# Kernel tuning notes

Measured on AMD Instinct MI355X. Metric: run time of the kernel, lower is better.

## Reference

```python
import jax, jax.numpy as jnp
import numpy as np

# --- SLAYER params (nmnistNet.yaml) ---
THETA = 10.0
TS = 1.0
TAU_REF = 1.0
SCALE_REF = 2.0
T_SAMPLE = 300
B = 8

def _alpha_kernel(tau, mult, t_sample, ts, eps=0.01):
    vals = []
    t = 0.0
    while t < t_sample:
        v = mult * t / tau * np.exp(1.0 - t / tau)
        if abs(v) < eps and t > tau:
            break
        vals.append(v)
        t += ts
    return np.asarray(vals, np.float32)

# refractory kernel: alpha kernel with mult = -scaleRef*theta (slayer._calculateRefKernel)
REF_KERNEL = _alpha_kernel(TAU_REF, -SCALE_REF * THETA, T_SAMPLE, TS)
NREF = REF_KERNEL.shape[0]  # 11 for these params; REF_KERNEL[0] == 0


def spike(u):
    """slayerCuda.getSpikes: per-neuron sequential threshold recurrence over time.
    u: [..., T] membrane potential. On spike at t, REF_KERNEL is accumulated
    into u[t:t+NREF]; spike amplitude is 1/Ts."""
    uT = jnp.moveaxis(u, -1, 0)  # [T, ...]
    refk = jnp.asarray(REF_KERNEL[1:]).reshape((NREF - 1,) + (1,) * (u.ndim - 1))
    buf0 = jnp.zeros((NREF - 1,) + uT.shape[1:], u.dtype)  # pending refractory

    def step(buf, u_t):
        u_mod = u_t + buf[0]
        ev = (u_mod >= THETA).astype(u.dtype)
        buf = jnp.concatenate([buf[1:], jnp.zeros_like(buf[:1])], axis=0) + ev[None] * refk
        return buf, ev / TS

    _, s = jax.lax.scan(step, buf0, uT)
    return jnp.moveaxis(s, 0, -1)


def conv2d_t(x, w, pad):
    """slayer.conv: Conv3d with kernel (k,k,1) == per-timestep 2D conv.
    x: [B,C,H,W,T], w: [O,I,kh,kw]."""
    b, c, h, wd, t = x.shape
    xb = jnp.moveaxis(x, -1, 1).reshape(b * t, c, h, wd)
    y = jax.lax.conv_general_dilated(xb, w, (1, 1), [(pad, pad), (pad, pad)],
                                     dimension_numbers=('NCHW', 'OIHW', 'NCHW'))
    o, ho, wo = y.shape[1], y.shape[2], y.shape[3]
    return jnp.moveaxis(y.reshape(b, t, o, ho, wo), 1, -1)


def sum_pool2(x):
    """slayer.pool(2): fixed-weight (1.1*theta) 2x2/stride-2 sum over H,W per channel."""
    y = jax.lax.reduce_window(x, 0.0, jax.lax.add, (1, 1, 2, 2, 1), (1, 1, 2, 2, 1), 'VALID')
    return 1.1 * THETA * y


def setup_inputs():
    key = jax.random.key(0)
    k0, k1, k2, k3, k4 = jax.random.split(key, 5)
    spikeInput = (jax.random.uniform(k0, (B, 2, 34, 34, T_SAMPLE)) < 0.1).astype(jnp.float32) / TS
    # conv weights: kaiming-uniform bound * 100 (the __init__ scales conv weights by 100)
    w1 = jax.random.uniform(k1, (16, 2, 5, 5), minval=-14.1, maxval=14.1, dtype=jnp.float32)
    w2 = jax.random.uniform(k2, (32, 16, 3, 3), minval=-8.3, maxval=8.3, dtype=jnp.float32)
    w3 = jax.random.uniform(k3, (64, 32, 3, 3), minval=-5.9, maxval=5.9, dtype=jnp.float32)
    wfc = jax.random.uniform(k4, (10, 64, 8, 8), minval=-0.5, maxval=0.5, dtype=jnp.float32)
    return {"spikeInput": spikeInput, "w1": w1, "w2": w2, "w3": w3, "wfc": wfc}


def reference(spikeInput, w1, w2, w3, wfc):
    s1 = spike(conv2d_t(spikeInput, w1, 1))  # [B,16,32,32,T]
    s2 = spike(sum_pool2(s1))                # [B,16,16,16,T]
    s3 = spike(conv2d_t(s2, w2, 1))          # [B,32,16,16,T]
    s4 = spike(sum_pool2(s3))                # [B,32,8,8,T]
    s5 = spike(conv2d_t(s4, w3, 1))          # [B,64,8,8,T]
    # dense((8,8,64),10): Conv3d(64,10,(8,8,1)) == full-spatial contraction
    u = jnp.einsum('bchwt,ochw->bot', s5, wfc)[:, :, None, None, :]
    return spike(u)                          # [B,10,1,1,T]
```

## Files before the change

kernel.cpp:

```cpp
#include <hip/hip_runtime.h>
#include <hip/hip_bf16.h>
#include <cmath>

#define T_SAMPLE 300
#define NCHUNK 75

typedef __attribute__((ext_vector_type(8))) short short8;
typedef __attribute__((ext_vector_type(4))) float f32x4;

struct RefK { float v[10]; };

__device__ __forceinline__ unsigned char spike_step(float u, float* buf, const RefK& rk) {
    const float um = u + buf[0];
    const bool fire = um >= 10.0f;
    const float ev = fire ? 1.0f : 0.0f;
#pragma unroll
    for (int r = 0; r < 9; ++r) buf[r] = fmaf(ev, rk.v[r], buf[r + 1]);
    buf[9] = ev * rk.v[9];
    return fire ? (unsigned char)1 : (unsigned char)0;
}

__device__ __forceinline__ short8 bytes_to_bf16x8(uint2 w8) {
    union { uint4 u; short8 s8; } cv;
    cv.u.x = (w8.x & 0xFFu) * 0x3F80u | ((((w8.x >> 8) & 0xFFu) * 0x3F80u) << 16);
    cv.u.y = ((w8.x >> 16) & 0xFFu) * 0x3F80u | ((((w8.x >> 24) & 0xFFu) * 0x3F80u) << 16);
    cv.u.z = (w8.y & 0xFFu) * 0x3F80u | ((((w8.y >> 8) & 0xFFu) * 0x3F80u) << 16);
    cv.u.w = ((w8.y >> 16) & 0xFFu) * 0x3F80u | ((((w8.y >> 24) & 0xFFu) * 0x3F80u) << 16);
    return cv.s8;
}

__device__ __forceinline__ unsigned short bf16_split_sel(float w, int s) {
    __hip_bfloat16 hb = __float2bfloat16(w);
    const float hf = __bfloat162float(hb);
    __hip_bfloat16 mb = __float2bfloat16(w - hf);
    const float mf = __bfloat162float(mb);
    __hip_bfloat16 lb = __float2bfloat16(w - hf - mf);
    __hip_bfloat16 sel = (s == 0) ? hb : ((s == 1) ? mb : lb);
    return *(unsigned short*)&sel;
}

__global__ __launch_bounds__(256) void transpose_in_k(
    const float* __restrict__ In, unsigned int* __restrict__ X)
{
    __shared__ unsigned int lds[16 * NCHUNK];
    const int blk = blockIdx.x;
    const int tn = threadIdx.x >> 4;
    const int tq = threadIdx.x & 15;
    const size_t n = (size_t)blk * 16 + tn;
#pragma unroll
    for (int p = 0; p < 5; ++p) {
        const int ch = p * 16 + tq;
        if (ch < NCHUNK) {
            const float4 v = *(const float4*)(In + n * T_SAMPLE + ch * 4);
            unsigned int u = (v.x != 0.f ? 1u : 0u) | (v.y != 0.f ? 0x100u : 0u) |
                             (v.z != 0.f ? 0x10000u : 0u) | (v.w != 0.f ? 0x1000000u : 0u);
            lds[tn * NCHUNK + ch] = u;
        }
    }
    __syncthreads();
    for (int idx = threadIdx.x; idx < 16 * NCHUNK; idx += 256) {
        const int ch = idx >> 4, t2 = idx & 15;
        X[(size_t)ch * 18496 + blk * 16 + t2] = lds[t2 * NCHUNK + ch];
    }
}

__global__ __launch_bounds__(256) void prep_w1_k(
    const float* __restrict__ w1, unsigned short* __restrict__ Wr1)
{
    const int g = blockIdx.x * 256 + threadIdx.x;
    const int j = g & 7;
    const int lane = (g >> 3) & 63;
    const int ks = (g >> 9) & 3;
    const int s = g >> 11;
    const int q = lane >> 4;
    const int oc = lane & 15;
    const int kg = ks * 32 + q * 8 + j;
    const int slot = kg >> 2, c = kg & 1;
    const int dy = slot / 6, dx = slot % 6;
    const float w = (dy < 5 && dx < 5) ? w1[((oc * 2 + c) * 5 + dy) * 5 + dx] * 0.5f : 0.f;
    Wr1[g] = bf16_split_sel(w, s);
}

__global__ __launch_bounds__(256) void prep_w3_k(
    const float* __restrict__ w3, unsigned short* __restrict__ Wr)
{
    const int g = blockIdx.x * 256 + threadIdx.x;
    const int j = g & 7;
    const int lane = (g >> 3) & 63;
    const int mt = (g >> 9) & 3;
    const int rest = g >> 11;
    const int ks = rest % 9;
    const int s = rest / 9;
    const int oc = mt * 16 + (lane & 15);
    const int ic = (lane >> 4) * 8 + j;
    Wr[g] = bf16_split_sel(w3[(oc * 32 + ic) * 9 + ks], s);
}

__global__ __launch_bounds__(256) void prep_w2_k(
    const float* __restrict__ w2, unsigned short* __restrict__ Wr2)
{
    const int g = blockIdx.x * 256 + threadIdx.x;
    const int j = g & 7;
    const int lane = (g >> 3) & 63;
    const int mt = (g >> 9) & 1;
    const int rest = g >> 10;
    const int kp = rest % 5;
    const int s = rest / 5;
    const int q = lane >> 4;
    const int oc = mt * 16 + (lane & 15);
    const int tap = kp * 2 + (q >> 1);
    const int ic = (q & 1) * 8 + j;
    const float w = (tap <= 8) ? w2[(oc * 16 + ic) * 9 + tap] : 0.f;
    Wr2[g] = bf16_split_sel(w, s);
}

__device__ __forceinline__ void c1_mfma_chunk(
    const unsigned int* __restrict__ tb, const int* offA, const int* offB,
    const short8* Af, f32x4* acc)
{
    unsigned int vA[4][4], vB[4][4];
#pragma unroll
    for (int ks = 0; ks < 4; ++ks)
#pragma unroll
        for (int t = 0; t < 4; ++t) {
            vA[ks][t] = tb[t * 72 + offA[ks]];
            vB[ks][t] = tb[t * 72 + offB[ks]];
        }

#pragma unroll
    for (int t = 0; t < 4; ++t) acc[t] = (f32x4){0.f, 0.f, 0.f, 0.f};
#pragma unroll
    for (int ks = 0; ks < 4; ++ks)
#pragma unroll
        for (int t = 0; t < 4; ++t) {
            union { uint4 u; short8 s8; } cv;
            cv.u.x = vA[ks][t]; cv.u.y = vA[ks][t];
            cv.u.z = vB[ks][t]; cv.u.w = vB[ks][t];
#pragma unroll
            for (int s = 0; s < 3; ++s)
                acc[t] = __builtin_amdgcn_mfma_f32_16x16x32_bf16(
                    Af[s * 4 + ks], cv.s8, acc[t], 0, 0, 0);
        }
}

__device__ __forceinline__ void c1_spike_store(
    const f32x4* acc, float (*buf)[10], const RefK& rk,
    uchar4* __restrict__ S1, int ch, int nb0)
{
#pragma unroll
    for (int rr = 0; rr < 4; ++rr) {
        uchar4 o;
        o.x = spike_step(acc[0][rr], buf[rr], rk);
        o.y = spike_step(acc[1][rr], buf[rr], rk);
        o.z = spike_step(acc[2][rr], buf[rr], rk);
        o.w = spike_step(acc[3][rr], buf[rr], rk);
        S1[(size_t)ch * 131072 + nb0 + rr * 1024] = o;
    }
}

__global__ __launch_bounds__(64) void conv1sp_k(
    const unsigned int* __restrict__ X, const unsigned short* __restrict__ Wr1,
    uchar4* __restrict__ S1, RefK rk)
{
    __shared__ unsigned int tab[25 * 4 * 72];
    const int pg = blockIdx.x;
    const int b = blockIdx.y;
    const int ty = pg >> 2, tx = pg & 3;
    const int lane = threadIdx.x;
    const int q = lane >> 4, n = lane & 15;
    const int py0 = n >> 3, px0 = n & 7;

    short8 Af[12];
#pragma unroll
    for (int s = 0; s < 3; ++s)
#pragma unroll
        for (int ks = 0; ks < 4; ++ks)
            Af[s * 4 + ks] = *(const short8*)(Wr1 + (((s * 4 + ks) * 64 + lane) * 8));

    int offA[4], offB[4];
#pragma unroll
    for (int ks = 0; ks < 4; ++ks) {
        const int sA = ks * 8 + q * 2, sB = sA + 1;
        const int dyA = sA / 6, dxA = sA - dyA * 6;
        const int dyB = sB / 6, dxB = sB - dyB * 6;
        offA[ks] = min(py0 + dyA, 5) * 12 + min(px0 + dxA, 11);
        offB[ks] = min(py0 + dyB, 5) * 12 + min(px0 + dxB, 11);
    }

    int lidx[29];
    int gof[29];
#pragma unroll
    for (int i = 0; i < 29; ++i) {
        const int e = i * 64 + lane;
        if (e < 1800) {
            const int chl = e / 72, site = e - chl * 72;
            const int r = site / 12, cc = site - r * 12;
            const int gy = ty * 2 - 1 + r, gx = tx * 8 - 1 + cc;
            lidx[i] = chl * 288 + site;
            gof[i] = (((unsigned)gy < 34u) && ((unsigned)gx < 34u))
                   ? (chl * 18496 + (b * 2) * 1156 + gy * 34 + gx) : -1;
        } else { lidx[i] = -1; gof[i] = -1; }
    }

    unsigned int w0[29], w1[29];
#pragma unroll
    for (int i = 0; i < 29; ++i) {
        if (gof[i] >= 0) { w0[i] = X[gof[i]]; w1[i] = X[gof[i] + 1156]; }
        else { w0[i] = 0u; w1[i] = 0u; }
    }

    float buf[4][10];
#pragma unroll
    for (int rr = 0; rr < 4; ++rr)
#pragma unroll
        for (int r = 0; r < 10; ++r) buf[rr][r] = 0.f;

    const int nb0 = (b * 16 + q * 4) * 1024 + (ty * 2 + py0) * 32 + tx * 8 + px0;

    f32x4 accA[4], accB[4];

    for (int st = 0; st < 3; ++st) {
#pragma unroll
        for (int i = 0; i < 29; ++i) {
            if (lidx[i] >= 0) {
#pragma unroll
                for (int t = 0; t < 4; ++t)
                    tab[lidx[i] + t * 72] =
                        ((w0[i] >> (8 * t)) & 0xFFu) * 0x3F80u
                        | ((((w1[i] >> (8 * t)) & 0xFFu) * 0x3F80u) << 16);
            }
        }
        __syncthreads();

        if (st < 2) {
            const unsigned int* Xs = X + (size_t)(st + 1) * (25 * 18496);
#pragma unroll
            for (int i = 0; i < 29; ++i) {
                if (gof[i] >= 0) { w0[i] = Xs[gof[i]]; w1[i] = Xs[gof[i] + 1156]; }
            }
        }

        const int ch0 = st * 25;
        c1_mfma_chunk(tab, offA, offB, Af, accA);
        for (int pp = 0; pp < 12; ++pp) {
            c1_mfma_chunk(tab + (2 * pp + 1) * 288, offA, offB, Af, accB);
            c1_spike_store(accA, buf, rk, S1, ch0 + 2 * pp, nb0);
            c1_mfma_chunk(tab + (2 * pp + 2) * 288, offA, offB, Af, accA);
            c1_spike_store(accB, buf, rk, S1, ch0 + 2 * pp + 1, nb0);
        }
        c1_spike_store(accA, buf, rk, S1, ch0 + 24, nb0);
        __syncthreads();
    }
}

__global__ __launch_bounds__(256) void conv2_mfma_k(
    const unsigned int* __restrict__ s2u, const unsigned short* __restrict__ Wr2,
    float4* __restrict__ U, int b0, int nbl)
{
    __shared__ __align__(16) unsigned char pad[4 * 18 * 18 * 16];
    const int tc = blockIdx.x;
    const int bl = blockIdx.z;
    const int b = b0 + bl;
    const int tid = threadIdx.x;
    const int wv = tid >> 6, lane = tid & 63;
    const int q = lane >> 4, n = lane & 15;
    const int PLANE_U = nbl * 8192;

    unsigned int* lp = (unsigned int*)pad;
    for (int i = tid; i < 5184; i += 256) lp[i] = 0u;
    __syncthreads();
    const unsigned int* sb = s2u + (size_t)tc * 32768 + b * 4096;
    for (int e = tid; e < 4096; e += 256) {
        const unsigned int v = sb[e];
        const int c = e >> 8, pix = e & 255;
        const int base = (((pix >> 4) + 1) * 18 + ((pix & 15) + 1)) * 16 + c;
        pad[base]         = (unsigned char)(v & 0xFFu);
        pad[5184 + base]  = (unsigned char)((v >> 8) & 0xFFu);
        pad[10368 + base] = (unsigned char)((v >> 16) & 0xFFu);
        pad[15552 + base] = (unsigned char)(v >> 24);
    }
    __syncthreads();

    for (int i = 0; i < 4; ++i) {
        const int r = wv * 4 + i;
        f32x4 acc[2][4];
#pragma unroll
        for (int mt = 0; mt < 2; ++mt)
#pragma unroll
            for (int t = 0; t < 4; ++t) acc[mt][t] = (f32x4){0.f, 0.f, 0.f, 0.f};

        for (int kp = 0; kp < 5; ++kp) {
            short8 Af[6];
#pragma unroll
            for (int s = 0; s < 3; ++s)
#pragma unroll
                for (int mt = 0; mt < 2; ++mt)
                    Af[s * 2 + mt] = *(const short8*)(Wr2 + ((((s * 5 + kp) * 2 + mt) * 64 + lane) * 8));
            int tap = kp * 2 + (q >> 1);
            if (tap > 8) tap = 8;
            const int dy = tap / 3, dx = tap % 3;
#pragma unroll
            for (int t = 0; t < 4; ++t) {
                const int off = ((t * 18 + r + dy) * 18 + (n + dx)) * 16 + (q & 1) * 8;
                const short8 Bf = bytes_to_bf16x8(*(const uint2*)(pad + off));
#pragma unroll
                for (int s = 0; s < 3; ++s)
#pragma unroll
                    for (int mt = 0; mt < 2; ++mt)
                        acc[mt][t] = __builtin_amdgcn_mfma_f32_16x16x32_bf16(
                            Af[s * 2 + mt], Bf, acc[mt][t], 0, 0, 0);
            }
        }

        const size_t ub = (size_t)tc * PLANE_U;
#pragma unroll
        for (int mt = 0; mt < 2; ++mt)
#pragma unroll
            for (int rr = 0; rr < 4; ++rr) {
                const int oc = mt * 16 + q * 4 + rr;
                const int nb = (bl * 32 + oc) * 256 + r * 16 + n;
                U[ub + nb] = make_float4(acc[mt][0][rr], acc[mt][1][rr], acc[mt][2][rr], acc[mt][3][rr]);
            }
    }
}

__global__ __launch_bounds__(256) void conv3_mfma_k(
    const unsigned int* __restrict__ s4u, const unsigned short* __restrict__ Wr,
    float4* __restrict__ U)
{
    __shared__ __align__(16) unsigned char pad[12800];
    const int tc = blockIdx.x;
    const int bl = blockIdx.z;
    const int tid = threadIdx.x;
    const int wv = tid >> 6, lane = tid & 63;
    const int q = lane >> 4, n = lane & 15;

    unsigned int* lp = (unsigned int*)pad;
    for (int i = tid; i < 3200; i += 256) lp[i] = 0u;
    __syncthreads();
    const unsigned int* sb = s4u + (size_t)tc * 16384 + bl * 2048;
    for (int e = tid; e < 2048; e += 256) {
        const unsigned int v = sb[e];
        const int c = e >> 6, pix = e & 63;
        const int base = (((pix >> 3) + 1) * 10 + ((pix & 7) + 1)) * 32 + c;
        pad[base]        = (unsigned char)(v & 0xFFu);
        pad[3200 + base] = (unsigned char)((v >> 8) & 0xFFu);
        pad[6400 + base] = (unsigned char)((v >> 16) & 0xFFu);
        pad[9600 + base] = (unsigned char)(v >> 24);
    }
    __syncthreads();

    const int pixel = wv * 16 + n;
    const int py0 = pixel >> 3, px0 = pixel & 7;

    f32x4 acc[4][4];
#pragma unroll
    for (int mt = 0; mt < 4; ++mt)
#pragma unroll
        for (int t = 0; t < 4; ++t) acc[mt][t] = (f32x4){0.f, 0.f, 0.f, 0.f};

    for (int ks = 0; ks < 9; ++ks) {
        const int dy = ks / 3, dx = ks % 3;
        short8 Af[12];
#pragma unroll
        for (int s = 0; s < 3; ++s)
#pragma unroll
            for (int mt = 0; mt < 4; ++mt)
                Af[s * 4 + mt] = *(const short8*)(Wr + ((((s * 9 + ks) * 4 + mt) * 64 + lane) * 8));
#pragma unroll
        for (int t = 0; t < 4; ++t) {
            const int off = ((t * 10 + py0 + dy) * 10 + (px0 + dx)) * 32 + q * 8;
            const short8 Bf = bytes_to_bf16x8(*(const uint2*)(pad + off));
#pragma unroll
            for (int s = 0; s < 3; ++s)
#pragma unroll
                for (int mt = 0; mt < 4; ++mt)
                    acc[mt][t] = __builtin_amdgcn_mfma_f32_16x16x32_bf16(
                        Af[s * 4 + mt], Bf, acc[mt][t], 0, 0, 0);
        }
    }

    const size_t ub = (size_t)tc * 32768 + (size_t)bl * 4096;
#pragma unroll
    for (int mt = 0; mt < 4; ++mt)
#pragma unroll
        for (int r = 0; r < 4; ++r) {
            const int oc = mt * 16 + q * 4 + r;
            const int nb = oc * 64 + wv * 16 + n;
            U[ub + nb] = make_float4(acc[mt][0][r], acc[mt][1][r], acc[mt][2][r], acc[mt][3][r]);
        }
}

__device__ __forceinline__ void spike_body(
    const float4* __restrict__ U, uchar4* __restrict__ S,
    int nneur, int sstride, int soff, const RefK& rk)
{
    const int n = blockIdx.x * 64 + threadIdx.x;
    const float4* up = U + n;
    uchar4* sp = S + soff + n;
    float buf[10];
#pragma unroll
    for (int r = 0; r < 10; ++r) buf[r] = 0.f;

    float4 ring[8];
#pragma unroll
    for (int r = 0; r < 8; ++r) ring[r] = up[(size_t)r * nneur];

#pragma unroll 8
    for (int ch = 0; ch < 72; ++ch) {
        const float4 cur = ring[ch & 7];
        const int pf = (ch + 8 < NCHUNK) ? ch + 8 : NCHUNK - 1;
        ring[ch & 7] = up[(size_t)pf * nneur];
        uchar4 o;
        o.x = spike_step(cur.x, buf, rk);
        o.y = spike_step(cur.y, buf, rk);
        o.z = spike_step(cur.z, buf, rk);
        o.w = spike_step(cur.w, buf, rk);
        sp[(size_t)ch * sstride] = o;
    }
#pragma unroll
    for (int ch = 72; ch < NCHUNK; ++ch) {
        const float4 cur = ring[ch & 7];
        uchar4 o;
        o.x = spike_step(cur.x, buf, rk);
        o.y = spike_step(cur.y, buf, rk);
        o.z = spike_step(cur.z, buf, rk);
        o.w = spike_step(cur.w, buf, rk);
        sp[(size_t)ch * sstride] = o;
    }
}

__global__ __launch_bounds__(64) void spike2_k(
    const float4* U, uchar4* S, int nneur, int sstride, int soff, RefK rk)
{ spike_body(U, S, nneur, sstride, soff, rk); }

__global__ __launch_bounds__(64) void spike3_k(
    const float4* U, uchar4* S, int nneur, int sstride, int soff, RefK rk)
{ spike_body(U, S, nneur, sstride, soff, rk); }

__device__ __forceinline__ int bsum4(uint2 r0, uint2 r1, int k) {
    return (int)((r0.x >> (8 * k)) & 0xffu) + (int)((r0.y >> (8 * k)) & 0xffu)
         + (int)((r1.x >> (8 * k)) & 0xffu) + (int)((r1.y >> (8 * k)) & 0xffu);
}

template <int C, int H, int W>
__device__ __forceinline__ void pool_body(
    const uchar4* __restrict__ Sin, uchar4* __restrict__ Sout, const RefK& rk)
{
    constexpr int H2 = H / 2, W2 = W / 2;
    constexpr int SIN = 8 * C * H * W;
    constexpr int SOUT = 8 * C * H2 * W2;
    const int n = blockIdx.x * 64 + threadIdx.x;
    const int x = n % W2;
    const int y = (n / W2) % H2;
    const int c = (n / (W2 * H2)) % C;
    const int b = n / (W2 * H2 * C);
    const int base = (((b * C + c) * H + 2 * y) * W + 2 * x);
    uchar4* q = Sout + n;

    float buf[10];
#pragma unroll
    for (int r = 0; r < 10; ++r) buf[r] = 0.f;

    uint2 r0[8], r1[8];
#pragma unroll
    for (int r = 0; r < 8; ++r) {
        r0[r] = *(const uint2*)(Sin + (size_t)r * SIN + base);
        r1[r] = *(const uint2*)(Sin + (size_t)r * SIN + base + W);
    }

#pragma unroll 8
    for (int ch = 0; ch < 72; ++ch) {
        const uint2 a0 = r0[ch & 7], a1 = r1[ch & 7];
        const int pf = (ch + 8 < NCHUNK) ? ch + 8 : NCHUNK - 1;
        r0[ch & 7] = *(const uint2*)(Sin + (size_t)pf * SIN + base);
        r1[ch & 7] = *(const uint2*)(Sin + (size_t)pf * SIN + base + W);
        uchar4 o;
        o.x = spike_step(11.0f * (float)bsum4(a0, a1, 0), buf, rk);
        o.y = spike_step(11.0f * (float)bsum4(a0, a1, 1), buf, rk);
        o.z = spike_step(11.0f * (float)bsum4(a0, a1, 2), buf, rk);
        o.w = spike_step(11.0f * (float)bsum4(a0, a1, 3), buf, rk);
        q[(size_t)ch * SOUT] = o;
    }
#pragma unroll
    for (int ch = 72; ch < NCHUNK; ++ch) {
        const uint2 a0 = r0[ch & 7], a1 = r1[ch & 7];
        uchar4 o;
        o.x = spike_step(11.0f * (float)bsum4(a0, a1, 0), buf, rk);
        o.y = spike_step(11.0f * (float)bsum4(a0, a1, 1), buf, rk);
        o.z = spike_step(11.0f * (float)bsum4(a0, a1, 2), buf, rk);
        o.w = spike_step(11.0f * (float)bsum4(a0, a1, 3), buf, rk);
        q[(size_t)ch * SOUT] = o;
    }
}

__global__ __launch_bounds__(64) void pool2_k(
    const uchar4* Sin, uchar4* Sout, RefK rk) { pool_body<16, 32, 32>(Sin, Sout, rk); }
__global__ __launch_bounds__(64) void pool4_k(
    const uchar4* Sin, uchar4* Sout, RefK rk) { pool_body<32, 16, 16>(Sin, Sout, rk); }

__global__ __launch_bounds__(64) void dense_k(
    const uchar4* __restrict__ S5, const float* __restrict__ WFC,
    float4* __restrict__ U6)
{
    const int tc = blockIdx.x, o = blockIdx.y, b = blockIdx.z;
    const int lane = threadIdx.x;
    float a0 = 0.f, a1 = 0.f, a2 = 0.f, a3 = 0.f;
    const uchar4* sb = S5 + (size_t)tc * 32768 + b * 4096;
    const float* wb = WFC + o * 4096;
    for (int i = 0; i < 64; ++i) {
        const int site = i * 64 + lane;
        const uchar4 s = sb[site];
        const float w = wb[site];
        a0 = fmaf(w, (float)s.x, a0);
        a1 = fmaf(w, (float)s.y, a1);
        a2 = fmaf(w, (float)s.z, a2);
        a3 = fmaf(w, (float)s.w, a3);
    }
#pragma unroll
    for (int m = 1; m < 64; m <<= 1) {
        a0 += __shfl_xor(a0, m, 64);
        a1 += __shfl_xor(a1, m, 64);
        a2 += __shfl_xor(a2, m, 64);
        a3 += __shfl_xor(a3, m, 64);
    }
    if (lane == 0)
        U6[(size_t)tc * 80 + b * 10 + o] = make_float4(a0, a1, a2, a3);
}

__global__ __launch_bounds__(128) void spike6_k(
    const float4* __restrict__ U6, float* __restrict__ Out, RefK rk)
{
    const int n = threadIdx.x;
    if (n >= 80) return;
    const float4* up = U6 + n;
    float* op = Out + (size_t)n * T_SAMPLE;
    float buf[10];
#pragma unroll
    for (int r = 0; r < 10; ++r) buf[r] = 0.f;

    float4 ring[8];
#pragma unroll
    for (int r = 0; r < 8; ++r) ring[r] = up[(size_t)r * 80];

#pragma unroll 8
    for (int ch = 0; ch < 72; ++ch) {
        const float4 cur = ring[ch & 7];
        const int pf = (ch + 8 < NCHUNK) ? ch + 8 : NCHUNK - 1;
        ring[ch & 7] = up[(size_t)pf * 80];
        float4 o;
        o.x = (float)spike_step(cur.x, buf, rk);
        o.y = (float)spike_step(cur.y, buf, rk);
        o.z = (float)spike_step(cur.z, buf, rk);
        o.w = (float)spike_step(cur.w, buf, rk);
        *(float4*)(op + ch * 4) = o;
    }
#pragma unroll
    for (int ch = 72; ch < NCHUNK; ++ch) {
        const float4 cur = ring[ch & 7];
        float4 o;
        o.x = (float)spike_step(cur.x, buf, rk);
        o.y = (float)spike_step(cur.y, buf, rk);
        o.z = (float)spike_step(cur.z, buf, rk);
        o.w = (float)spike_step(cur.w, buf, rk);
        *(float4*)(op + ch * 4) = o;
    }
}

extern "C" void kernel_launch(void* const* d_in, const int* in_sizes, int n_in,
                              void* d_out, int out_size, void* d_ws, size_t ws_size,
                              hipStream_t stream)
{
    const float* spikeIn = (const float*)d_in[0];
    const float* w1 = (const float*)d_in[1];
    const float* w2 = (const float*)d_in[2];
    const float* w3 = (const float*)d_in[3];
    const float* wfc = (const float*)d_in[4];
    float* out = (float*)d_out;

    RefK rk;
    for (int t = 1; t <= 10; ++t)
        rk.v[t - 1] = (float)(-20.0 * (double)t * std::exp(1.0 - (double)t));

    const size_t A_BYTES = 39321600;
    const size_t B_BYTES = 9830400;
    const size_t U6_BYTES = 96000;
    const size_t U_BIG = 78643200, U_SMALL = 39321600;
    const size_t TAIL = A_BYTES + B_BYTES + U6_BYTES;
    const bool big = ws_size >= U_BIG + TAIL;
    const size_t U_BYTES = big ? U_BIG : U_SMALL;

    char* ws = (char*)d_ws;
    float4* U = (float4*)ws;
    uchar4* A = (uchar4*)(ws + U_BYTES);
    uchar4* Bb = (uchar4*)(ws + U_BYTES + A_BYTES);
    float4* U6 = (float4*)(ws + U_BYTES + A_BYTES + B_BYTES);
    unsigned short* Wr = (unsigned short*)(ws + U_BYTES + 20971520);
    unsigned short* Wr2 = (unsigned short*)(ws + U_BYTES + 20971520 + 131072);
    unsigned short* Wr1 = (unsigned short*)(ws + U_BYTES + A_BYTES + 5570560);

    uchar4* X = Bb;
    uchar4* s1 = A;
    uchar4* s2 = Bb;
    uchar4* s3 = A;
    uchar4* s4 = Bb;
    uchar4* s5 = A;

    transpose_in_k<<<18496 / 16, 256, 0, stream>>>(spikeIn, (unsigned int*)X);
    prep_w1_k<<<24, 256, 0, stream>>>(w1, Wr1);

    {
        dim3 g1(64, 8);
        conv1sp_k<<<g1, 64, 0, stream>>>((const unsigned int*)X, Wr1, s1, rk);
    }
    pool2_k<<<32768 / 64, 64, 0, stream>>>(s1, s2, rk);
    prep_w2_k<<<60, 256, 0, stream>>>(w2, Wr2);
    prep_w3_k<<<216, 256, 0, stream>>>(w3, Wr);
    const int nbl2 = big ? 8 : 4;
    for (int b0 = 0; b0 < 8; b0 += nbl2) {
        dim3 g2(NCHUNK, 1, nbl2);
        conv2_mfma_k<<<g2, 256, 0, stream>>>((const unsigned int*)s2, Wr2, U, b0, nbl2);
        const int nn = nbl2 * 8192;
        spike2_k<<<nn / 64, 64, 0, stream>>>(U, s3, nn, 65536, b0 * 8192, rk);
    }
    pool4_k<<<16384 / 64, 64, 0, stream>>>(s3, s4, rk);
    {
        dim3 g3(NCHUNK, 1, 8);
        conv3_mfma_k<<<g3, 256, 0, stream>>>((const unsigned int*)s4, Wr, U);
        spike3_k<<<32768 / 64, 64, 0, stream>>>(U, s5, 32768, 32768, 0, rk);
    }
    dim3 g6(NCHUNK, 10, 8);
    dense_k<<<g6, 64, 0, stream>>>(s5, wfc, U6);
    spike6_k<<<1, 128, 0, stream>>>(U6, out, rk);
}
```

Measured before the change: 293.5 us.

## Split conv1 MFMA across four waves and stage potentials through LDS for spiking

The fused conv1+spike kernel grows from one wave to four waves per block. The waves share the MFMA work for 15-timestep-chunk windows and write membrane potentials to LDS. Each of the 256 threads then runs the sequential spike recurrence for one output neuron across the window. This trades the single-wave interleaving of MFMA and spiking for more parallel MFMA issue and higher occupancy. It adds extra LDS traffic, more barriers and larger shared memory per block, and the spike phase is no longer overlapped with MFMA.

```diff
diff --git a/kernel.cpp b/kernel.cpp
--- a/kernel.cpp
+++ b/kernel.cpp
@@ -143,30 +143,17 @@
         }
 }
 
-__device__ __forceinline__ void c1_spike_store(
-    const f32x4* acc, float (*buf)[10], const RefK& rk,
-    uchar4* __restrict__ S1, int ch, int nb0)
-{
-#pragma unroll
-    for (int rr = 0; rr < 4; ++rr) {
-        uchar4 o;
-        o.x = spike_step(acc[0][rr], buf[rr], rk);
-        o.y = spike_step(acc[1][rr], buf[rr], rk);
-        o.z = spike_step(acc[2][rr], buf[rr], rk);
-        o.w = spike_step(acc[3][rr], buf[rr], rk);
-        S1[(size_t)ch * 131072 + nb0 + rr * 1024] = o;
-    }
-}
-
-__global__ __launch_bounds__(64) void conv1sp_k(
+__global__ __launch_bounds__(256) void conv1ps_k(
     const unsigned int* __restrict__ X, const unsigned short* __restrict__ Wr1,
     uchar4* __restrict__ S1, RefK rk)
 {
-    __shared__ unsigned int tab[25 * 4 * 72];
+    __shared__ unsigned int tab[15 * 288];
+    __shared__ __align__(16) float4 Ulds[15 * 256];
     const int pg = blockIdx.x;
     const int b = blockIdx.y;
     const int ty = pg >> 2, tx = pg & 3;
-    const int lane = threadIdx.x;
+    const int tid = threadIdx.x;
+    const int wv = tid >> 6, lane = tid & 63;
     const int q = lane >> 4, n = lane & 15;
     const int py0 = n >> 3, px0 = n & 7;
 
@@ -187,12 +174,12 @@
         offB[ks] = min(py0 + dyB, 5) * 12 + min(px0 + dxB, 11);
     }
 
-    int lidx[29];
-    int gof[29];
-#pragma unroll
-    for (int i = 0; i < 29; ++i) {
-        const int e = i * 64 + lane;
-        if (e < 1800) {
+    int lidx[5];
+    int gof[5];
+#pragma unroll
+    for (int i = 0; i < 5; ++i) {
+        const int e = i * 256 + tid;
+        if (e < 1080) {
             const int chl = e / 72, site = e - chl * 72;
             const int r = site / 12, cc = site - r * 12;
             const int gy = ty * 2 - 1 + r, gx = tx * 8 - 1 + cc;
@@ -202,26 +189,22 @@
         } else { lidx[i] = -1; gof[i] = -1; }
     }
 
-    unsigned int w0[29], w1[29];
-#pragma unroll
-    for (int i = 0; i < 29; ++i) {
+    unsigned int w0[5], w1[5];
+#pragma unroll
+    for (int i = 0; i < 5; ++i) {
         if (gof[i] >= 0) { w0[i] = X[gof[i]]; w1[i] = X[gof[i] + 1156]; }
         else { w0[i] = 0u; w1[i] = 0u; }
     }
 
-    float buf[4][10];
-#pragma unroll
-    for (int rr = 0; rr < 4; ++rr)
-#pragma unroll
-        for (int r = 0; r < 10; ++r) buf[rr][r] = 0.f;
-
-    const int nb0 = (b * 16 + q * 4) * 1024 + (ty * 2 + py0) * 32 + tx * 8 + px0;
-
-    f32x4 accA[4], accB[4];
-
-    for (int st = 0; st < 3; ++st) {
-#pragma unroll
-        for (int i = 0; i < 29; ++i) {
+    float buf[10];
+#pragma unroll
+    for (int r = 0; r < 10; ++r) buf[r] = 0.f;
+    const int s_oc = tid >> 4, s_n = tid & 15;
+    const int nb0 = (b * 16 + s_oc) * 1024 + (ty * 2 + (s_n >> 3)) * 32 + tx * 8 + (s_n & 7);
+
+    for (int w = 0; w < 5; ++w) {
+#pragma unroll
+        for (int i = 0; i < 5; ++i) {
             if (lidx[i] >= 0) {
 #pragma unroll
                 for (int t = 0; t < 4; ++t)
@@ -232,24 +215,33 @@
         }
         __syncthreads();
 
-        if (st < 2) {
-            const unsigned int* Xs = X + (size_t)(st + 1) * (25 * 18496);
-#pragma unroll
-            for (int i = 0; i < 29; ++i) {
+        for (int k = wv; k < 15; k += 4) {
+            f32x4 acc[4];
+            c1_mfma_chunk(tab + k * 288, offA, offB, Af, acc);
+#pragma unroll
+            for (int rr = 0; rr < 4; ++rr)
+                Ulds[k * 256 + (q * 4 + rr) * 16 + n] =
+                    make_float4(acc[0][rr], acc[1][rr], acc[2][rr], acc[3][rr]);
+        }
+        __syncthreads();
+
+        if (w < 4) {
+            const unsigned int* Xs = X + (size_t)(w + 1) * (15 * 18496);
+#pragma unroll
+            for (int i = 0; i < 5; ++i) {
                 if (gof[i] >= 0) { w0[i] = Xs[gof[i]]; w1[i] = Xs[gof[i] + 1156]; }
             }
         }
 
-        const int ch0 = st * 25;
-        c1_mfma_chunk(tab, offA, offB, Af, accA);
-        for (int pp = 0; pp < 12; ++pp) {
-            c1_mfma_chunk(tab + (2 * pp + 1) * 288, offA, offB, Af, accB);
-            c1_spike_store(accA, buf, rk, S1, ch0 + 2 * pp, nb0);
-            c1_mfma_chunk(tab + (2 * pp + 2) * 288, offA, offB, Af, accA);
-            c1_spike_store(accB, buf, rk, S1, ch0 + 2 * pp + 1, nb0);
-        }
-        c1_spike_store(accA, buf, rk, S1, ch0 + 24, nb0);
-        __syncthreads();
+        for (int k = 0; k < 15; ++k) {
+            const float4 u = Ulds[k * 256 + tid];
+            uchar4 o;
+            o.x = spike_step(u.x, buf, rk);
+            o.y = spike_step(u.y, buf, rk);
+            o.z = spike_step(u.z, buf, rk);
+            o.w = spike_step(u.w, buf, rk);
+            S1[(size_t)(w * 15 + k) * 131072 + nb0] = o;
+        }
     }
 }
 
@@ -611,7 +603,7 @@
 
     {
         dim3 g1(64, 8);
-        conv1sp_k<<<g1, 64, 0, stream>>>((const unsigned int*)X, Wr1, s1, rk);
+        conv1ps_k<<<g1, 256, 0, stream>>>((const unsigned int*)X, Wr1, s1, rk);
     }
     pool2_k<<<32768 / 64, 64, 0, stream>>>(s1, s2, rk);
     prep_w2_k<<<60, 256, 0, stream>>>(w2, Wr2);
```

Result: faster. 259.3 us (-11.7%).
